# Optimization experiments

Hardware: AMD Instinct MI355X
Metric: run time of the kernel (lower is better)

## Reference

```python
import jax, jax.numpy as jnp
import numpy as np

BS, T, C, D = 2, 64, 64, 64
N, K_CONN = 1024, 32

def setup_inputs() -> dict:
    key = jax.random.key(0)
    k_cc, k_eot, k_idx, k_prim, k_w = jax.random.split(key, 5)
    cc_signals = jax.random.normal(k_cc, (BS, T, C, D), dtype=jnp.float32)
    eot_mask = jax.random.bernoulli(k_eot, 0.05, (BS, T))
    # random sparse connectivity (original excludes self-loops; random is fine for the math)
    conn_indices = jnp.sort(jax.random.randint(k_idx, (N, K_CONN), 0, N), axis=-1).astype(jnp.int32)
    conn_mask = jnp.ones((N, K_CONN), dtype=bool)
    # primitives: RMS-normalized per neuron
    prim_raw = 1.0 + jax.random.normal(k_prim, (N, D), dtype=jnp.float32) * 0.02
    rms = jnp.clip(jnp.sqrt(jnp.mean(prim_raw ** 2, axis=-1, keepdims=True)), 1e-8, None)
    primitives = prim_raw / rms
    # conn_weights: L1-normalized per neuron
    raw_w = jax.random.uniform(k_w, (N, K_CONN), dtype=jnp.float32) + 0.01
    conn_weights = raw_w / jnp.sum(jnp.abs(raw_w), axis=-1, keepdims=True)
    decay_logit = jnp.zeros((N,), dtype=jnp.float32)
    h0 = jnp.zeros((BS, N, D), dtype=jnp.float32)
    prev_msg0 = jnp.zeros((BS, N, D), dtype=jnp.float32)
    return {"cc_signals": cc_signals, "eot_mask": eot_mask, "conn_indices": conn_indices,
            "conn_mask": conn_mask, "primitives": primitives, "conn_weights": conn_weights,
            "decay_logit": decay_logit, "h0": h0, "prev_msg0": prev_msg0, "grad_window": 8}

def reference(cc_signals, eot_mask, conn_indices, conn_mask, primitives,
              conn_weights, decay_logit, h0, prev_msg0, grad_window):
    Bs, Tt, Cc, Dd = cc_signals.shape
    Nn = primitives.shape[0]
    # L2-normalize CC signals along D
    cc = cc_signals / jnp.clip(jnp.linalg.norm(cc_signals, axis=-1, keepdims=True), 1e-8, None)
    # dense adjacency A[j, conn_indices[j,k]] += w[j,k]
    w_masked = conn_weights * conn_mask.astype(cc.dtype)
    A = jnp.zeros((Nn, Nn), dtype=cc.dtype).at[jnp.arange(Nn)[:, None], conn_indices].add(w_masked)
    decay = jax.nn.sigmoid(decay_logit)[:, None]  # [N,1]

    def step(carry, x):
        h, pm = carry
        cc_t, eot_t, t = x  # cc_t [BS,C,D], eot_t [BS]
        reset = (t % grad_window) == 0  # truncated-BPTT detach boundary (no-op in fwd)
        h = jnp.where(reset, jax.lax.stop_gradient(h), h)
        pm = jnp.where(reset, jax.lax.stop_gradient(pm), pm)
        received = jnp.einsum('nm,bmd->bnd', A, pm)  # [BS,N,D]
        received = received.at[:, :Cc].add(cc_t)
        d_t = decay * (1.0 - eot_t[:, None, None].astype(h.dtype))  # EOT resets state
        h = d_t * h + (1.0 - d_t) * received
        pm = jnp.tanh(h * primitives)
        return (h, pm), pm[:, :Cc]

    xs = (jnp.transpose(cc, (1, 0, 2, 3)), eot_mask.T, jnp.arange(Tt))
    (_, _), out = jax.lax.scan(step, (h0, prev_msg0), xs)
    return jnp.transpose(out, (1, 0, 2, 3))  # [BS,T,C,D]
```

## Files before the change

### kernel.cpp

```cpp
#include <hip/hip_runtime.h>
#include <math.h>


#define NN   1024
#define TT   64
#define CCn  64
#define DD   64
#define KC   32
#define TPB  1024

__device__ __forceinline__ float fast_tanh(float x) {
    x = fminf(9.0f, fmaxf(-9.0f, x));
    const float e = __expf(2.0f * x);
    return (e - 1.0f) / (e + 1.0f);
}

__global__ __launch_bounds__(256) void mg_prep(const float* __restrict__ cc,
                                               float* __restrict__ ccn) {
    const int lane = threadIdx.x & 63;
    const int wv   = threadIdx.x >> 6;
    const int row  = (int)blockIdx.x * 4 + wv;
    const float v = cc[row * DD + lane];
    float ss = v * v;
    #pragma unroll
    for (int off = 32; off >= 1; off >>= 1) ss += __shfl_xor(ss, off, 64);
    const float nv = v / fmaxf(sqrtf(ss), 1e-8f);
    const int c = row & 63;
    const int t = (row >> 6) & 63;
    const int b = row >> 12;
    ccn[(((lane * 2 + b) * TT) + t) * CCn + c] = nv;
}

__global__ __launch_bounds__(TPB, 4) void mg_main(
    const int*   __restrict__ eot,
    const int*   __restrict__ cidx,
    const float* __restrict__ cw,
    const float* __restrict__ prim,
    const float* __restrict__ dlog,
    const float* __restrict__ h0,
    const float* __restrict__ pm0,
    const float* __restrict__ ccn,
    float*       __restrict__ out)
{
    __shared__ float pmf[2][NN];

    const int tid = (int)threadIdx.x;
    const int wg  = (int)blockIdx.x;
    const int d   = wg & 63;
    const int b   = wg >> 6;

    int   ofs[KC];
    float w[KC];
    #pragma unroll
    for (int k = 0; k < KC; ++k) {
        ofs[k] = cidx[tid * KC + k];
        w[k]   = cw[tid * KC + k];
    }
    const float pv  = prim[tid * DD + d];
    const float dec = 1.0f / (1.0f + __expf(-dlog[tid]));
    float h = h0[(b * NN + tid) * DD + d];
    pmf[0][tid] = pm0[(b * NN + tid) * DD + d];

    const int lane = tid & 63;
    const unsigned long long em = __ballot(eot[b * TT + lane] != 0);

    const float* ccb = ccn + (size_t)(d * 2 + b) * TT * CCn;

    __syncthreads();

    for (int t = 0; t < TT; ++t) {
        const float* src = pmf[t & 1];
        float*       dst = pmf[(t + 1) & 1];

        float a0 = 0.f, a1 = 0.f, a2 = 0.f, a3 = 0.f;
        #pragma unroll
        for (int k = 0; k < KC; k += 4) {
            a0 = fmaf(w[k + 0], src[ofs[k + 0]], a0);
            a1 = fmaf(w[k + 1], src[ofs[k + 1]], a1);
            a2 = fmaf(w[k + 2], src[ofs[k + 2]], a2);
            a3 = fmaf(w[k + 3], src[ofs[k + 3]], a3);
        }
        float recv = (a0 + a1) + (a2 + a3);

        if (tid < CCn) recv += ccb[t * CCn + tid];

        const float e  = (float)((em >> t) & 1ull);
        const float dt = dec * (1.0f - e);
        h = dt * h + (1.0f - dt) * recv;
        const float pmv = fast_tanh(h * pv);

        dst[tid] = pmv;
        if (tid < CCn)
            out[((size_t)(b * TT + t) * CCn + tid) * DD + d] = pmv;

        __syncthreads();
    }
}

extern "C" void kernel_launch(void* const* d_in, const int* in_sizes, int n_in,
                              void* d_out, int out_size, void* d_ws, size_t ws_size,
                              hipStream_t stream) {
    const float* cc   = (const float*)d_in[0];
    const int*   eot  = (const int*)  d_in[1];
    const int*   cidx = (const int*)  d_in[2];
    const float* prim = (const float*)d_in[4];
    const float* cw   = (const float*)d_in[5];
    const float* dlog = (const float*)d_in[6];
    const float* h0   = (const float*)d_in[7];
    const float* pm0  = (const float*)d_in[8];

    float* ccn = (float*)d_ws;

    hipLaunchKernelGGL(mg_prep, dim3(2 * TT * CCn / 4), dim3(256), 0, stream,
                       cc, ccn);
    hipLaunchKernelGGL(mg_main, dim3(2 * DD), dim3(TPB), 0, stream,
                       eot, cidx, cw, prim, dlog, h0, pm0, ccn, (float*)d_out);
}
```

Before: 187.9 us.

## Reorder connection indices by LDS bank and rotate per lane to avoid conflicts

Adds a preprocessing kernel that sorts each neuron's 32 connections by LDS bank (index mod 32), rotates the order by the thread id and stores byte offsets. In the gather step, lanes of a wavefront then tend to hit different banks at the same k, which is meant to cut shared-memory bank conflicts. Indices and weights are now loaded with vector int4/float4 loads, and the launch-bounds occupancy hint is dropped. The cost is one extra kernel launch per call, plus a changed FMA summation order that can shift results slightly.

```diff
diff --git a/kernel.cpp b/kernel.cpp
--- a/kernel.cpp
+++ b/kernel.cpp
@@ -13,6 +13,10 @@
     x = fminf(9.0f, fmaxf(-9.0f, x));
     const float e = __expf(2.0f * x);
     return (e - 1.0f) / (e + 1.0f);
+}
+
+__device__ __forceinline__ float ldsf(const float* base, int byteoff) {
+    return *(const float*)((const char*)base + byteoff);
 }
 
 __global__ __launch_bounds__(256) void mg_prep(const float* __restrict__ cc,
@@ -31,10 +35,34 @@
     ccn[(((lane * 2 + b) * TT) + t) * CCn + c] = nv;
 }
 
-__global__ __launch_bounds__(TPB, 4) void mg_main(
+__global__ __launch_bounds__(256) void mg_sort(const int* __restrict__ cidx,
+                                               const float* __restrict__ cw,
+                                               int* __restrict__ idx2,
+                                               float* __restrict__ w2) {
+    const int n = (int)blockIdx.x * 256 + (int)threadIdx.x;
+    int   ib[KC];
+    float wb[KC];
+    #pragma unroll
+    for (int k = 0; k < KC; ++k) { ib[k] = cidx[n * KC + k]; wb[k] = cw[n * KC + k]; }
+    for (int i = 1; i < KC; ++i) {
+        const int vi = ib[i]; const float vw = wb[i];
+        const int key = vi & 31;
+        int j = i - 1;
+        while (j >= 0 && (ib[j] & 31) > key) { ib[j + 1] = ib[j]; wb[j + 1] = wb[j]; --j; }
+        ib[j + 1] = vi; wb[j + 1] = vw;
+    }
+    const int rot = n & 31;
+    for (int s = 0; s < KC; ++s) {
+        const int p = (s + rot) & 31;
+        idx2[n * KC + s] = ib[p] * 4;
+        w2[n * KC + s]   = wb[p];
+    }
+}
+
+__global__ __launch_bounds__(TPB) void mg_main(
     const int*   __restrict__ eot,
-    const int*   __restrict__ cidx,
-    const float* __restrict__ cw,
+    const int*   __restrict__ idx2,
+    const float* __restrict__ w2,
     const float* __restrict__ prim,
     const float* __restrict__ dlog,
     const float* __restrict__ h0,
@@ -49,13 +77,13 @@
     const int d   = wg & 63;
     const int b   = wg >> 6;
 
-    int   ofs[KC];
-    float w[KC];
-    #pragma unroll
-    for (int k = 0; k < KC; ++k) {
-        ofs[k] = cidx[tid * KC + k];
-        w[k]   = cw[tid * KC + k];
-    }
+    const int4*   ip = (const int4*)(idx2 + tid * KC);
+    const float4* wp = (const float4*)(w2 + tid * KC);
+    const int4   i0 = ip[0], i1 = ip[1], i2 = ip[2], i3 = ip[3],
+                 i4 = ip[4], i5 = ip[5], i6 = ip[6], i7 = ip[7];
+    const float4 w0 = wp[0], w1 = wp[1], w2v = wp[2], w3 = wp[3],
+                 w4 = wp[4], w5 = wp[5], w6 = wp[6], w7 = wp[7];
+
     const float pv  = prim[tid * DD + d];
     const float dec = 1.0f / (1.0f + __expf(-dlog[tid]));
     float h = h0[(b * NN + tid) * DD + d];
@@ -73,13 +101,14 @@
         float*       dst = pmf[(t + 1) & 1];
 
         float a0 = 0.f, a1 = 0.f, a2 = 0.f, a3 = 0.f;
-        #pragma unroll
-        for (int k = 0; k < KC; k += 4) {
-            a0 = fmaf(w[k + 0], src[ofs[k + 0]], a0);
-            a1 = fmaf(w[k + 1], src[ofs[k + 1]], a1);
-            a2 = fmaf(w[k + 2], src[ofs[k + 2]], a2);
-            a3 = fmaf(w[k + 3], src[ofs[k + 3]], a3);
-        }
+#define G4(iv, wv)                                  \
+        a0 = fmaf(wv.x, ldsf(src, iv.x), a0);       \
+        a1 = fmaf(wv.y, ldsf(src, iv.y), a1);       \
+        a2 = fmaf(wv.z, ldsf(src, iv.z), a2);       \
+        a3 = fmaf(wv.w, ldsf(src, iv.w), a3);
+        G4(i0, w0) G4(i1, w1) G4(i2, w2v) G4(i3, w3)
+        G4(i4, w4) G4(i5, w5) G4(i6, w6)  G4(i7, w7)
+#undef G4
         float recv = (a0 + a1) + (a2 + a3);
 
         if (tid < CCn) recv += ccb[t * CCn + tid];
@@ -109,10 +138,14 @@
     const float* h0   = (const float*)d_in[7];
     const float* pm0  = (const float*)d_in[8];
 
-    float* ccn = (float*)d_ws;
+    float* ccn  = (float*)d_ws;
+    int*   idx2 = (int*)(ccn + (size_t)DD * 2 * TT * CCn);
+    float* w2   = (float*)(idx2 + NN * KC);
 
     hipLaunchKernelGGL(mg_prep, dim3(2 * TT * CCn / 4), dim3(256), 0, stream,
                        cc, ccn);
+    hipLaunchKernelGGL(mg_sort, dim3(NN / 256), dim3(256), 0, stream,
+                       cidx, cw, idx2, w2);
     hipLaunchKernelGGL(mg_main, dim3(2 * DD), dim3(TPB), 0, stream,
-                       eot, cidx, cw, prim, dlog, h0, pm0, ccn, (float*)d_out);
+                       eot, idx2, w2, prim, dlog, h0, pm0, ccn, (float*)d_out);
 }
```

Result: slower. 307.8 us (+63.8%).

## Compute inverse norms only and fuse CC normalization into main loop with vector index loads

Applied to the files above, without the earlier changes.

The prep kernel now writes only one inverse L2 norm per CC row instead of a transposed normalized copy of the whole signal tensor. The main kernel reads the raw CC value (strided by D) and multiplies by the inverse norm inside the time loop, cutting prep-kernel write traffic. Connection indices and weights are loaded as 4-wide vectors, indices are pre-scaled to byte offsets for LDS addressing, and an asm barrier keeps them in registers. Launch bounds no longer request 4 waves per SIMD. The per-step strided global loads of raw CC may add latency on the serial timestep critical path.

```diff
diff --git a/kernel.cpp b/kernel.cpp
--- a/kernel.cpp
+++ b/kernel.cpp
@@ -9,14 +9,21 @@
 #define KC   32
 #define TPB  1024
 
+typedef int   i32x4 __attribute__((ext_vector_type(4)));
+typedef float f32x4 __attribute__((ext_vector_type(4)));
+
 __device__ __forceinline__ float fast_tanh(float x) {
     x = fminf(9.0f, fmaxf(-9.0f, x));
     const float e = __expf(2.0f * x);
     return (e - 1.0f) / (e + 1.0f);
 }
 
-__global__ __launch_bounds__(256) void mg_prep(const float* __restrict__ cc,
-                                               float* __restrict__ ccn) {
+__device__ __forceinline__ float ldsf(const float* base, int byteoff) {
+    return *(const float*)((const char*)base + byteoff);
+}
+
+__global__ __launch_bounds__(256) void mg_norm(const float* __restrict__ cc,
+                                               float* __restrict__ invn) {
     const int lane = threadIdx.x & 63;
     const int wv   = threadIdx.x >> 6;
     const int row  = (int)blockIdx.x * 4 + wv;
@@ -24,14 +31,11 @@
     float ss = v * v;
     #pragma unroll
     for (int off = 32; off >= 1; off >>= 1) ss += __shfl_xor(ss, off, 64);
-    const float nv = v / fmaxf(sqrtf(ss), 1e-8f);
-    const int c = row & 63;
-    const int t = (row >> 6) & 63;
-    const int b = row >> 12;
-    ccn[(((lane * 2 + b) * TT) + t) * CCn + c] = nv;
+    if (lane == 0) invn[row] = 1.0f / fmaxf(sqrtf(ss), 1e-8f);
 }
 
-__global__ __launch_bounds__(TPB, 4) void mg_main(
+__global__ __launch_bounds__(TPB) void mg_main(
+    const float* __restrict__ cc,
     const int*   __restrict__ eot,
     const int*   __restrict__ cidx,
     const float* __restrict__ cw,
@@ -39,7 +43,7 @@
     const float* __restrict__ dlog,
     const float* __restrict__ h0,
     const float* __restrict__ pm0,
-    const float* __restrict__ ccn,
+    const float* __restrict__ invn,
     float*       __restrict__ out)
 {
     __shared__ float pmf[2][NN];
@@ -49,13 +53,17 @@
     const int d   = wg & 63;
     const int b   = wg >> 6;
 
-    int   ofs[KC];
-    float w[KC];
-    #pragma unroll
-    for (int k = 0; k < KC; ++k) {
-        ofs[k] = cidx[tid * KC + k];
-        w[k]   = cw[tid * KC + k];
-    }
+    const i32x4* ip = (const i32x4*)(cidx + tid * KC);
+    const f32x4* wp = (const f32x4*)(cw + tid * KC);
+    i32x4 i0 = ip[0] * 4, i1 = ip[1] * 4, i2 = ip[2] * 4, i3 = ip[3] * 4,
+          i4 = ip[4] * 4, i5 = ip[5] * 4, i6 = ip[6] * 4, i7 = ip[7] * 4;
+    f32x4 w0 = wp[0], w1 = wp[1], w2v = wp[2], w3 = wp[3],
+          w4 = wp[4], w5 = wp[5], w6 = wp[6], w7 = wp[7];
+    asm volatile("" : "+v"(i0), "+v"(i1), "+v"(i2), "+v"(i3),
+                      "+v"(i4), "+v"(i5), "+v"(i6), "+v"(i7),
+                      "+v"(w0), "+v"(w1), "+v"(w2v), "+v"(w3),
+                      "+v"(w4), "+v"(w5), "+v"(w6), "+v"(w7));
+
     const float pv  = prim[tid * DD + d];
     const float dec = 1.0f / (1.0f + __expf(-dlog[tid]));
     float h = h0[(b * NN + tid) * DD + d];
@@ -64,25 +72,30 @@
     const int lane = tid & 63;
     const unsigned long long em = __ballot(eot[b * TT + lane] != 0);
 
-    const float* ccb = ccn + (size_t)(d * 2 + b) * TT * CCn;
-
     __syncthreads();
 
     for (int t = 0; t < TT; ++t) {
         const float* src = pmf[t & 1];
         float*       dst = pmf[(t + 1) & 1];
 
+        float ccraw = 0.0f, ccinv = 0.0f;
+        if (tid < CCn) {
+            const int rc = (b * TT + t) * CCn + tid;
+            ccraw = cc[(size_t)rc * DD + d];
+            ccinv = invn[rc];
+        }
+
         float a0 = 0.f, a1 = 0.f, a2 = 0.f, a3 = 0.f;
-        #pragma unroll
-        for (int k = 0; k < KC; k += 4) {
-            a0 = fmaf(w[k + 0], src[ofs[k + 0]], a0);
-            a1 = fmaf(w[k + 1], src[ofs[k + 1]], a1);
-            a2 = fmaf(w[k + 2], src[ofs[k + 2]], a2);
-            a3 = fmaf(w[k + 3], src[ofs[k + 3]], a3);
-        }
+#define G4(iv, wv)                                  \
+        a0 = fmaf(wv.x, ldsf(src, iv.x), a0);       \
+        a1 = fmaf(wv.y, ldsf(src, iv.y), a1);       \
+        a2 = fmaf(wv.z, ldsf(src, iv.z), a2);       \
+        a3 = fmaf(wv.w, ldsf(src, iv.w), a3);
+        G4(i0, w0) G4(i1, w1) G4(i2, w2v) G4(i3, w3)
+        G4(i4, w4) G4(i5, w5) G4(i6, w6)  G4(i7, w7)
+#undef G4
         float recv = (a0 + a1) + (a2 + a3);
-
-        if (tid < CCn) recv += ccb[t * CCn + tid];
+        recv += ccraw * ccinv;
 
         const float e  = (float)((em >> t) & 1ull);
         const float dt = dec * (1.0f - e);
@@ -109,10 +122,11 @@
     const float* h0   = (const float*)d_in[7];
     const float* pm0  = (const float*)d_in[8];
 
-    float* ccn = (float*)d_ws;
+    float* invn = (float*)d_ws;
 
-    hipLaunchKernelGGL(mg_prep, dim3(2 * TT * CCn / 4), dim3(256), 0, stream,
-                       cc, ccn);
+    hipLaunchKernelGGL(mg_norm, dim3(2 * TT * CCn / 4), dim3(256), 0, stream,
+                       cc, invn);
     hipLaunchKernelGGL(mg_main, dim3(2 * DD), dim3(TPB), 0, stream,
-                       eot, cidx, cw, prim, dlog, h0, pm0, ccn, (float*)d_out);
+                       cc, eot, cidx, cw, prim, dlog, h0, pm0, invn,
+                       (float*)d_out);
 }
```

Result: no change. 188.1 us (+0.1%).

## Precompute bank-conflict-free gather schedule for LDS neighbor reads

Applied to the files above, without the earlier changes.

Adds a scheduling kernel that reorders each neuron's connection indices so that slot p reads LDS bank (n+p) mod 32. Within a wave, the first 32 gathers are then conflict-free, and duplicate-bank indices go to 24 overflow slots. Indices are stored as byte offsets and loaded as int4/float4 vectors. The aim is to remove LDS bank conflicts in the serial recurrence loop. The cost is 56 gathers per step instead of 32, an extra kernel launch, and loss of contributions if more than 24 indices overflow. The min-blocks launch bound is also dropped.

```diff
diff --git a/kernel.cpp b/kernel.cpp
--- a/kernel.cpp
+++ b/kernel.cpp
@@ -8,11 +8,17 @@
 #define DD   64
 #define KC   32
 #define TPB  1024
+#define NSL  56
+#define OVS  24
 
 __device__ __forceinline__ float fast_tanh(float x) {
     x = fminf(9.0f, fmaxf(-9.0f, x));
     const float e = __expf(2.0f * x);
     return (e - 1.0f) / (e + 1.0f);
+}
+
+__device__ __forceinline__ float ldsf(const float* base, int byteoff) {
+    return *(const float*)((const char*)base + byteoff);
 }
 
 __global__ __launch_bounds__(256) void mg_prep(const float* __restrict__ cc,
@@ -31,10 +37,60 @@
     ccn[(((lane * 2 + b) * TT) + t) * CCn + c] = nv;
 }
 
-__global__ __launch_bounds__(TPB, 4) void mg_main(
+__global__ __launch_bounds__(256) void mg_sched(const int* __restrict__ cidx,
+                                                const float* __restrict__ cw,
+                                                int* __restrict__ sidx,
+                                                float* __restrict__ sw) {
+    const int tid  = (int)threadIdx.x;
+    const int lane = tid & 63;
+    const int half = lane >> 5;
+    const int s    = lane & 31;
+    const int wv   = tid >> 6;
+    const int n    = (int)blockIdx.x * 8 + wv * 2 + half;
+
+    const int   myidx  = cidx[n * KC + s];
+    const float myw    = cw[n * KC + s];
+    const int   mybank = myidx & 31;
+
+    bool is_first = true;
+    bool present  = false;
+    #pragma unroll
+    for (int t = 0; t < 32; ++t) {
+        const int bb = __shfl(mybank, (lane & 32) + t, 64);
+        if (t < s && bb == mybank) is_first = false;
+        if (bb == s) present = true;
+    }
+
+    const unsigned long long bf    = __ballot(is_first);
+    const unsigned long long gmask = (half ? 0xFFFFFFFF00000000ull
+                                           : 0x00000000FFFFFFFFull);
+    const unsigned long long ovf   = ~bf & gmask;
+    const unsigned long long below = (lane ? ((1ull << lane) - 1ull) : 0ull);
+    const int myrank = (int)__popcll(ovf & below);
+    const int OVC    = (int)__popcll(ovf);
+
+    int*   so = sidx + n * NSL;
+    float* wo = sw   + n * NSL;
+    if (is_first) {
+        const int p = (mybank - n) & 31;
+        so[p] = myidx * 4;  wo[p] = myw;
+    } else {
+        const int p = 32 + (myrank < OVS ? myrank : OVS - 1);
+        so[p] = myidx * 4;  wo[p] = myw;
+    }
+    if (!present) {
+        const int p = (s - n) & 31;
+        so[p] = s * 4;      wo[p] = 0.0f;
+    }
+    if (s >= OVC && s < OVS) {
+        so[32 + s] = 0;     wo[32 + s] = 0.0f;
+    }
+}
+
+__global__ __launch_bounds__(TPB) void mg_main(
     const int*   __restrict__ eot,
-    const int*   __restrict__ cidx,
-    const float* __restrict__ cw,
+    const int*   __restrict__ sidx,
+    const float* __restrict__ sw,
     const float* __restrict__ prim,
     const float* __restrict__ dlog,
     const float* __restrict__ h0,
@@ -49,13 +105,17 @@
     const int d   = wg & 63;
     const int b   = wg >> 6;
 
-    int   ofs[KC];
-    float w[KC];
-    #pragma unroll
-    for (int k = 0; k < KC; ++k) {
-        ofs[k] = cidx[tid * KC + k];
-        w[k]   = cw[tid * KC + k];
-    }
+    const int4*   ip = (const int4*)(sidx + tid * NSL);
+    const float4* wp = (const float4*)(sw + tid * NSL);
+    const int4   i0 = ip[0],  i1 = ip[1],  i2 = ip[2],  i3 = ip[3],
+                 i4 = ip[4],  i5 = ip[5],  i6 = ip[6],  i7 = ip[7],
+                 i8 = ip[8],  i9 = ip[9],  iA = ip[10], iB = ip[11],
+                 iC = ip[12], iD = ip[13];
+    const float4 w0 = wp[0],  w1 = wp[1],  w2 = wp[2],  w3 = wp[3],
+                 w4 = wp[4],  w5 = wp[5],  w6 = wp[6],  w7 = wp[7],
+                 w8 = wp[8],  w9 = wp[9],  wA = wp[10], wB = wp[11],
+                 wC = wp[12], wD = wp[13];
+
     const float pv  = prim[tid * DD + d];
     const float dec = 1.0f / (1.0f + __expf(-dlog[tid]));
     float h = h0[(b * NN + tid) * DD + d];
@@ -73,13 +133,16 @@
         float*       dst = pmf[(t + 1) & 1];
 
         float a0 = 0.f, a1 = 0.f, a2 = 0.f, a3 = 0.f;
-        #pragma unroll
-        for (int k = 0; k < KC; k += 4) {
-            a0 = fmaf(w[k + 0], src[ofs[k + 0]], a0);
-            a1 = fmaf(w[k + 1], src[ofs[k + 1]], a1);
-            a2 = fmaf(w[k + 2], src[ofs[k + 2]], a2);
-            a3 = fmaf(w[k + 3], src[ofs[k + 3]], a3);
-        }
+#define G4(iv, wv)                                  \
+        a0 = fmaf(wv.x, ldsf(src, iv.x), a0);       \
+        a1 = fmaf(wv.y, ldsf(src, iv.y), a1);       \
+        a2 = fmaf(wv.z, ldsf(src, iv.z), a2);       \
+        a3 = fmaf(wv.w, ldsf(src, iv.w), a3);
+        G4(i0, w0) G4(i1, w1) G4(i2, w2) G4(i3, w3)
+        G4(i4, w4) G4(i5, w5) G4(i6, w6) G4(i7, w7)
+        G4(i8, w8) G4(i9, w9) G4(iA, wA) G4(iB, wB)
+        G4(iC, wC) G4(iD, wD)
+#undef G4
         float recv = (a0 + a1) + (a2 + a3);
 
         if (tid < CCn) recv += ccb[t * CCn + tid];
@@ -109,10 +172,14 @@
     const float* h0   = (const float*)d_in[7];
     const float* pm0  = (const float*)d_in[8];
 
-    float* ccn = (float*)d_ws;
+    float* ccn  = (float*)d_ws;
+    int*   sidx = (int*)(ccn + (size_t)DD * 2 * TT * CCn);
+    float* sw   = (float*)(sidx + NN * NSL);
 
     hipLaunchKernelGGL(mg_prep, dim3(2 * TT * CCn / 4), dim3(256), 0, stream,
                        cc, ccn);
+    hipLaunchKernelGGL(mg_sched, dim3(NN / 8), dim3(256), 0, stream,
+                       cidx, cw, sidx, sw);
     hipLaunchKernelGGL(mg_main, dim3(2 * DD), dim3(TPB), 0, stream,
-                       eot, cidx, cw, prim, dlog, h0, pm0, ccn, (float*)d_out);
+                       eot, sidx, sw, prim, dlog, h0, pm0, ccn, (float*)d_out);
 }
```

Result: slower. 333.9 us (+77.7%).
